# Optimization experiments

Measured on AMD Instinct MI355X. Metric: run time of the kernel, lower is better.

Reference implementation:

```python
import jax, jax.numpy as jnp
import numpy as np

B, N = 8, 2048
HYPER, IN_F, OUT_F = 128, 64, 64
ALPHA = 0.2  # LeakyReLU negative slope
NEG_INF = -9e15


def setup_inputs() -> dict:
    key = jax.random.key(0)
    k1, k2, k3, k4, k5, k6 = jax.random.split(key, 6)
    state = jax.random.normal(k1, (B, HYPER), dtype=jnp.float32)
    h = jax.random.normal(k2, (B, N, IN_F), dtype=jnp.float32)
    adj = jax.random.randint(k3, (B, N, N), 0, 2, dtype=jnp.int32)
    # hypernetwork linear: weight [in*out, hyper] (torch layout), bias [in*out]
    lim = 1.0 / np.sqrt(HYPER)
    Wp_w = jax.random.uniform(k4, (IN_F * OUT_F, HYPER), minval=-lim, maxval=lim, dtype=jnp.float32)
    Wp_b = jax.random.uniform(k5, (IN_F * OUT_F,), minval=-lim, maxval=lim, dtype=jnp.float32)
    # attention vector a [2*out, 1], xavier_uniform gain=1.414
    ga = 1.414 * np.sqrt(6.0 / (2 * OUT_F + 1))
    a = jax.random.uniform(k6, (2 * OUT_F, 1), minval=-ga, maxval=ga, dtype=jnp.float32)
    return {"state": state, "h": h, "adj": adj, "Wp_w": Wp_w, "Wp_b": Wp_b, "a": a}


def reference(state, h, adj, Wp_w, Wp_b, a):
    # hypernetwork-generated weight: abs(Linear(state)) -> [B, in, out]
    W = jnp.abs(state @ Wp_w.T + Wp_b).reshape(-1, IN_F, OUT_F)
    Wh = jnp.einsum('bni,bio->bno', h, W)          # [B, N, out]
    Wh1 = Wh @ a[:OUT_F, :]                        # [B, N, 1]
    Wh2 = Wh @ a[OUT_F:, :]                        # [B, N, 1]
    e = jax.nn.leaky_relu(Wh1 + jnp.transpose(Wh2, (0, 2, 1)), negative_slope=ALPHA)  # [B, N, N]
    scores = jnp.where(adj > 0, e, NEG_INF)
    attention = jax.nn.softmax(scores, axis=1)     # softmax over dim=1 as in original
    h_prime = jnp.einsum('bmn,bmo->bno', jnp.transpose(attention, (0, 2, 1)), Wh) if False else attention @ Wh
    return jax.nn.elu(h_prime)                     # concat=True
```

## Files before the change

### kernel.cpp

```cpp
#include <hip/hip_runtime.h>
#include <hip/hip_bf16.h>
#include <hip/hip_fp16.h>

#define B_ 8
#define N_ 2048
#define ALPHA_ 0.2f
#define LOG2E_ 1.44269504088896f

#define OFF_WB    0u
#define OFF_WA1   65536u
#define OFF_WA2   67584u
#define OFF_WH1   69632u
#define OFF_WH2   135168u
#define OFF_DEN   200704u
#define OFF_WHBT  266240u
#define OFF_MASK  2363392u

typedef _Float16 half8_t __attribute__((ext_vector_type(8)));
typedef float f32x4_t __attribute__((ext_vector_type(4)));
union UH { unsigned u[4]; half8_t s; };

__device__ __forceinline__ unsigned pkh(float a, float b) {
  __half2 h = __floats2half2_rn(a, b);
  return *(unsigned*)&h;
}
__device__ __forceinline__ unsigned pk2(float lo, float hi) {
  return ((__float_as_uint(hi) + 0x8000u) & 0xFFFF0000u) |
         ((__float_as_uint(lo) + 0x8000u) >> 16);
}

__global__ __launch_bounds__(256) void k1_hyperw(
    const float* __restrict__ state, const float* __restrict__ Wpw,
    const float* __restrict__ Wpb, const float* __restrict__ av,
    unsigned short* __restrict__ Wb, float* __restrict__ Wa1,
    float* __restrict__ Wa2) {
  int b = blockIdx.y;
  int r = blockIdx.x * 256 + threadIdx.x;
  int lane = threadIdx.x & 63;
  int i = r >> 6, o = r & 63;
  __shared__ float st[128];
  if (threadIdx.x < 128) st[threadIdx.x] = state[b * 128 + threadIdx.x];
  __syncthreads();
  float acc = Wpb[r];
  const float4* wp = (const float4*)(Wpw + (size_t)r * 128);
  #pragma unroll 8
  for (int hh = 0; hh < 32; ++hh) {
    float4 v = wp[hh];
    acc += st[hh*4]*v.x + st[hh*4+1]*v.y + st[hh*4+2]*v.z + st[hh*4+3]*v.w;
  }
  float wv = fabsf(acc);
  __half hw = __float2half(wv);
  Wb[b * 4096 + o * 64 + i] = *(unsigned short*)&hw;
  float p1 = wv * av[lane];
  float p2 = wv * av[64 + lane];
  #pragma unroll
  for (int off = 32; off > 0; off >>= 1) {
    p1 += __shfl_xor(p1, off);
    p2 += __shfl_xor(p2, off);
  }
  if (lane == 0) { Wa1[b * 64 + i] = p1; Wa2[b * 64 + i] = p2; }
}

__global__ __launch_bounds__(256) void k2_wh(
    const float* __restrict__ h, const unsigned short* __restrict__ Wb,
    const float* __restrict__ Wa1, const float* __restrict__ Wa2,
    float* __restrict__ Wh1, float* __restrict__ Wh2,
    unsigned short* __restrict__ WhbT) {
  int b = blockIdx.y;
  int tid = threadIdx.x, lane = tid & 63;
  int w = tid >> 6;
  int n0 = blockIdx.x * 64 + w * 16;
  int l15 = lane & 15, kg = lane >> 4;
  int row = n0 + l15;
  const float* hrow = h + (((size_t)b * N_ + row) << 6);
  float4 ha0 = *(const float4*)(hrow + kg * 8);
  float4 ha1 = *(const float4*)(hrow + kg * 8 + 4);
  float4 hb0 = *(const float4*)(hrow + 32 + kg * 8);
  float4 hb1 = *(const float4*)(hrow + 32 + kg * 8 + 4);
  const float* wa1 = Wa1 + b * 64;
  const float* wa2 = Wa2 + b * 64;
  float4 A0 = *(const float4*)(wa1 + kg * 8),      A1 = *(const float4*)(wa1 + kg * 8 + 4);
  float4 A2 = *(const float4*)(wa1 + 32 + kg * 8), A3 = *(const float4*)(wa1 + 32 + kg * 8 + 4);
  float4 C0 = *(const float4*)(wa2 + kg * 8),      C1 = *(const float4*)(wa2 + kg * 8 + 4);
  float4 C2 = *(const float4*)(wa2 + 32 + kg * 8), C3 = *(const float4*)(wa2 + 32 + kg * 8 + 4);
  float v1 = ha0.x*A0.x + ha0.y*A0.y + ha0.z*A0.z + ha0.w*A0.w
           + ha1.x*A1.x + ha1.y*A1.y + ha1.z*A1.z + ha1.w*A1.w
           + hb0.x*A2.x + hb0.y*A2.y + hb0.z*A2.z + hb0.w*A2.w
           + hb1.x*A3.x + hb1.y*A3.y + hb1.z*A3.z + hb1.w*A3.w;
  float v2 = ha0.x*C0.x + ha0.y*C0.y + ha0.z*C0.z + ha0.w*C0.w
           + ha1.x*C1.x + ha1.y*C1.y + ha1.z*C1.z + ha1.w*C1.w
           + hb0.x*C2.x + hb0.y*C2.y + hb0.z*C2.z + hb0.w*C2.w
           + hb1.x*C3.x + hb1.y*C3.y + hb1.z*C3.z + hb1.w*C3.w;
  v1 += __shfl_xor(v1, 16); v1 += __shfl_xor(v1, 32);
  v2 += __shfl_xor(v2, 16); v2 += __shfl_xor(v2, 32);
  if (lane < 16) {
    Wh1[b * N_ + row] = v1 * LOG2E_;
    Wh2[b * N_ + row] = v2 * LOG2E_;
  }
  UH ua, ub;
  ua.u[0] = pkh(ha0.x, ha0.y); ua.u[1] = pkh(ha0.z, ha0.w);
  ua.u[2] = pkh(ha1.x, ha1.y); ua.u[3] = pkh(ha1.z, ha1.w);
  ub.u[0] = pkh(hb0.x, hb0.y); ub.u[1] = pkh(hb0.z, hb0.w);
  ub.u[2] = pkh(hb1.x, hb1.y); ub.u[3] = pkh(hb1.z, hb1.w);
  const unsigned short* wbb = Wb + b * 4096;
  f32x4_t acc[4];
  #pragma unroll
  for (int of = 0; of < 4; ++of) acc[of] = {0.f, 0.f, 0.f, 0.f};
  #pragma unroll
  for (int of = 0; of < 4; ++of) {
    int o = of * 16 + l15;
    half8_t b0 = *(const half8_t*)(wbb + o * 64 + kg * 8);
    half8_t b1 = *(const half8_t*)(wbb + o * 64 + 32 + kg * 8);
    acc[of] = __builtin_amdgcn_mfma_f32_16x16x32_f16(ua.s, b0, acc[of], 0, 0, 0);
    acc[of] = __builtin_amdgcn_mfma_f32_16x16x32_f16(ub.s, b1, acc[of], 0, 0, 0);
  }
  int nb = n0 + (kg << 2);
  #pragma unroll
  for (int of = 0; of < 4; ++of) {
    int o = of * 16 + l15;
    uint2 pk;
    pk.x = pkh(acc[of][0], acc[of][1]);
    pk.y = pkh(acc[of][2], acc[of][3]);
    *(uint2*)(WhbT + ((size_t)(b * 64 + o)) * N_ + nb) = pk;
  }
}

#define K3_PROC(VV, UVV, II)                                                 \
  do {                                                                       \
    bool p0 = (VV).x > 0, p1 = (VV).y > 0, p2 = (VV).z > 0, p3 = (VV).w > 0; \
    unsigned long long b0 = __ballot(p0), b1 = __ballot(p1);                 \
    unsigned long long b2 = __ballot(p2), b3 = __ballot(p3);                 \
    unsigned long long bsel = qsel == 0 ? b0 : qsel == 1 ? b1                \
                            : qsel == 2 ? b2 : b3;                           \
    wreg = (rsel == (II)) ? bsel : wreg;                                     \
    den0 += p0 ? fmaxf((UVV).x, (UVV).y * b2c0) : 0.f;                       \
    den1 += p1 ? fmaxf((UVV).x, (UVV).y * b2c1) : 0.f;                       \
    den2 += p2 ? fmaxf((UVV).x, (UVV).y * b2c2) : 0.f;                       \
    den3 += p3 ? fmaxf((UVV).x, (UVV).y * b2c3) : 0.f;                       \
  } while (0)

__global__ __launch_bounds__(256) void k3_mask(
    const int* __restrict__ adj, const float* __restrict__ Wh1,
    const float* __restrict__ Wh2, float* __restrict__ den,
    unsigned long long* __restrict__ maskQ) {
  int jg = blockIdx.x, ic = blockIdx.y, b = blockIdx.z;
  int tid = threadIdx.x, lane = tid & 63, w = tid >> 6;
  int i0 = ic * 64 + w * 16;
  __shared__ float2 uvs[64];
  __shared__ float red[4][256];
  if (tid < 64) {
    float w1v = Wh1[b * N_ + ic * 64 + tid];
    uvs[tid] = make_float2(exp2f(w1v), exp2f(0.2f * w1v));
  }
  __syncthreads();
  float2 uv0 = uvs[(w<<4)+0],  uv1 = uvs[(w<<4)+1],  uv2 = uvs[(w<<4)+2],  uv3 = uvs[(w<<4)+3];
  float2 uv4 = uvs[(w<<4)+4],  uv5 = uvs[(w<<4)+5],  uv6 = uvs[(w<<4)+6],  uv7 = uvs[(w<<4)+7];
  float2 uv8 = uvs[(w<<4)+8],  uv9 = uvs[(w<<4)+9],  uvA = uvs[(w<<4)+10], uvB = uvs[(w<<4)+11];
  float2 uvC = uvs[(w<<4)+12], uvD = uvs[(w<<4)+13], uvE = uvs[(w<<4)+14], uvF = uvs[(w<<4)+15];
  int j0 = jg * 256 + 4 * lane;
  float4 wh2v = *(const float4*)(Wh2 + b * N_ + j0);
  float b2c0 = exp2f(-0.8f * wh2v.x), b2c1 = exp2f(-0.8f * wh2v.y);
  float b2c2 = exp2f(-0.8f * wh2v.z), b2c3 = exp2f(-0.8f * wh2v.w);
  const int4* ap = (const int4*)(adj + ((size_t)(b * N_ + i0)) * N_ + jg * 256);
  const size_t rs = N_ / 4;
  int qsel = lane & 3, rsel = lane >> 2;
  unsigned long long wreg = 0;
  float den0 = 0.f, den1 = 0.f, den2 = 0.f, den3 = 0.f;
  int4 r0 = ap[0 * rs + lane], r1 = ap[1 * rs + lane];
  int4 r2 = ap[2 * rs + lane], r3 = ap[3 * rs + lane];
  int4 r4 = ap[4 * rs + lane], r5 = ap[5 * rs + lane];
  int4 r6 = ap[6 * rs + lane], r7 = ap[7 * rs + lane];
  K3_PROC(r0, uv0, 0);  r0 = ap[8 * rs + lane];
  K3_PROC(r1, uv1, 1);  r1 = ap[9 * rs + lane];
  K3_PROC(r2, uv2, 2);  r2 = ap[10 * rs + lane];
  K3_PROC(r3, uv3, 3);  r3 = ap[11 * rs + lane];
  K3_PROC(r4, uv4, 4);  r4 = ap[12 * rs + lane];
  K3_PROC(r5, uv5, 5);  r5 = ap[13 * rs + lane];
  K3_PROC(r6, uv6, 6);  r6 = ap[14 * rs + lane];
  K3_PROC(r7, uv7, 7);  r7 = ap[15 * rs + lane];
  K3_PROC(r0, uv8, 8);  K3_PROC(r1, uv9, 9);  K3_PROC(r2, uvA, 10); K3_PROC(r3, uvB, 11);
  K3_PROC(r4, uvC, 12); K3_PROC(r5, uvD, 13); K3_PROC(r6, uvE, 14); K3_PROC(r7, uvF, 15);
  maskQ[((((size_t)b * 8 + jg) * 2048 + i0 + rsel) << 2) + qsel] = wreg;
  red[w][(lane << 2) + 0] = den0;
  red[w][(lane << 2) + 1] = den1;
  red[w][(lane << 2) + 2] = den2;
  red[w][(lane << 2) + 3] = den3;
  __syncthreads();
  float dsum = red[0][tid] + red[1][tid] + red[2][tid] + red[3][tid];
  atomicAdd(den + b * N_ + jg * 256 + tid, dsum);
}

__global__ __launch_bounds__(512) void k4_mfma(
    const unsigned long long* __restrict__ maskQ, const float* __restrict__ Wh1,
    const float* __restrict__ Wh2, const float* __restrict__ den,
    const unsigned short* __restrict__ WhbT, float* __restrict__ out) {
  int ib = blockIdx.x, b = blockIdx.y;
  int tid = threadIdx.x, lane = tid & 63;
  int w = __builtin_amdgcn_readfirstlane(tid >> 6);
  int iw = w & 3, kh = w >> 2;
  extern __shared__ __align__(16) unsigned char smem[];
  unsigned* abL = (unsigned*)(smem + 32768);
  const unsigned short* wsrc = WhbT + (size_t)b * 64 * N_;
  int sl1 = 512 + tid, sl2 = 1024 + tid, sl3 = 1536 + tid;
  int h0 = 0, h1 = 0, h2 = 1, h3 = 1;
  int o0 = tid >> 4, o1 = (sl1 & 1023) >> 4, o2 = (sl2 & 1023) >> 4, o3 = (sl3 & 1023) >> 4;
  int s0 = tid & 15, s1 = sl1 & 15, s2 = sl2 & 15, s3 = sl3 & 15;
  uint4 sv0, sv1, sv2, sv3;
#define SLOAD(RR)                                                               \
  { sv0 = *(const uint4*)(wsrc + (size_t)o0 * N_ + h0 * 1024 + (RR) * 128 + s0 * 8); \
    sv1 = *(const uint4*)(wsrc + (size_t)o1 * N_ + h1 * 1024 + (RR) * 128 + s1 * 8); \
    sv2 = *(const uint4*)(wsrc + (size_t)o2 * N_ + h2 * 1024 + (RR) * 128 + s2 * 8); \
    sv3 = *(const uint4*)(wsrc + (size_t)o3 * N_ + h3 * 1024 + (RR) * 128 + s3 * 8); }
#define SWRITE()                                                                \
  { *(uint4*)(smem + h0 * 16384 + o0 * 256 + ((s0 * 16) ^ ((o0 & 7) << 4))) = sv0; \
    *(uint4*)(smem + h1 * 16384 + o1 * 256 + ((s1 * 16) ^ ((o1 & 7) << 4))) = sv1; \
    *(uint4*)(smem + h2 * 16384 + o2 * 256 + ((s2 * 16) ^ ((o2 & 7) << 4))) = sv2; \
    *(uint4*)(smem + h3 * 16384 + o3 * 256 + ((s3 * 16) ^ ((o3 & 7) << 4))) = sv3; }
  SLOAD(0)
  #pragma unroll
  for (int q = 0; q < 4; ++q) {
    int j = (q << 9) + tid;
    float dv = den[b * N_ + j];
    float inv = 1.0f / fmaxf(dv, 1e-37f);
    float B4 = exp2f(-0.8f * Wh2[b * N_ + j]) * inv;
    abL[j] = pk2(B4, inv);
  }
  SWRITE()
  int l15 = lane & 15, lg = lane >> 4;
  int i0 = (ib << 6) + (iw << 4);
  int i = i0 + l15;
  float w1 = Wh1[b * N_ + i];
  float u = exp2f(w1), v = exp2f(0.2f * w1);
  f32x4_t acc[4];
  #pragma unroll
  for (int of = 0; of < 4; ++of) acc[of] = {0.f, 0.f, 0.f, 0.f};
  unsigned char* mybt = smem + kh * 16384;
  const unsigned long long* mbase = maskQ + (size_t)b * 8 * 2048 * 4;
  for (int rr = 0; rr < 8; ++rr) {
    __syncthreads();
    if (rr < 7) SLOAD(rr + 1)
    int tg = kh * 8 + rr;
    int jg = tg >> 1, r2 = tg & 1;
    const uint4* qp = (const uint4*)(mbase + (((size_t)jg * 2048 + i) << 2));
    uint4 q0 = qp[0], q1 = qp[1];
    unsigned long long Wq[4];
    Wq[0] = ((unsigned long long)q0.y << 32) | q0.x;
    Wq[1] = ((unsigned long long)q0.w << 32) | q0.z;
    Wq[2] = ((unsigned long long)q1.y << 32) | q1.x;
    Wq[3] = ((unsigned long long)q1.w << 32) | q1.z;
    #pragma unroll
    for (int jt2 = 0; jt2 < 2; ++jt2) {
      #pragma unroll
      for (int s = 0; s < 2; ++s) {
        int jfull = kh * 1024 + rr * 128 + jt2 * 64 + s * 32 + lg * 8;
        int tbase = r2 * 32 + jt2 * 16 + s * 8 + lg * 2;
        unsigned m[4];
        #pragma unroll
        for (int k2 = 0; k2 < 4; ++k2)
          m[k2] = (unsigned)(Wq[k2] >> tbase) & 3u;
        const uint4* abp = (const uint4*)&abL[jfull];
        uint4 a0 = abp[0], a1 = abp[1];
        unsigned aw[8] = {a0.x, a0.y, a0.z, a0.w, a1.x, a1.y, a1.z, a1.w};
        UH A;
        #pragma unroll
        for (int p2 = 0; p2 < 4; ++p2) {
          int e0 = 2 * p2, e1 = 2 * p2 + 1;
          float A40 = __uint_as_float(aw[e0] & 0xFFFF0000u);
          float B40 = __uint_as_float(aw[e0] << 16);
          float A41 = __uint_as_float(aw[e1] & 0xFFFF0000u);
          float B41 = __uint_as_float(aw[e1] << 16);
          float plo = fmaxf(u * A40, v * B40);
          float phi = fmaxf(u * A41, v * B41);
          plo = (m[e0 & 3] & (1u << (e0 >> 2))) ? plo : 0.f;
          phi = (m[e1 & 3] & (1u << (e1 >> 2))) ? phi : 0.f;
          A.u[p2] = pkh(plo, phi);
        }
        int boff = jt2 * 128 + s * 64 + lg * 16;
        #pragma unroll
        for (int of = 0; of < 4; ++of) {
          int o = (of << 4) + l15;
          half8_t bv = *(const half8_t*)(mybt + o * 256 + (boff ^ ((o & 7) << 4)));
          acc[of] = __builtin_amdgcn_mfma_f32_16x16x32_f16(A.s, bv, acc[of], 0, 0, 0);
        }
      }
    }
    __syncthreads();
    if (rr < 7) SWRITE()
  }
  __syncthreads();
  float* fred = (float*)smem;
  if (kh == 1) {
    #pragma unroll
    for (int of = 0; of < 4; ++of)
      *(f32x4_t*)(fred + (((iw << 6) + lane) << 4) + (of << 2)) = acc[of];
  }
  __syncthreads();
  if (kh == 0) {
    #pragma unroll
    for (int of = 0; of < 4; ++of) {
      f32x4_t oth = *(const f32x4_t*)(fred + (((iw << 6) + lane) << 4) + (of << 2));
      #pragma unroll
      for (int q = 0; q < 4; ++q) {
        float xv = acc[of][q] + oth[q];
        xv = xv > 0.f ? xv : (__expf(xv) - 1.f);
        out[((size_t)(b * N_ + i0 + (lg << 2) + q)) * 64 + (of << 4) + l15] = xv;
      }
    }
  }
}

extern "C" void kernel_launch(void* const* d_in, const int* in_sizes, int n_in,
                              void* d_out, int out_size, void* d_ws, size_t ws_size,
                              hipStream_t stream) {
  const float* state = (const float*)d_in[0];
  const float* h     = (const float*)d_in[1];
  const int*   adj   = (const int*)d_in[2];
  const float* Wpw   = (const float*)d_in[3];
  const float* Wpb   = (const float*)d_in[4];
  const float* av    = (const float*)d_in[5];
  float* out = (float*)d_out;
  char* ws = (char*)d_ws;
  unsigned short* Wb = (unsigned short*)(ws + OFF_WB);
  float* Wa1  = (float*)(ws + OFF_WA1);
  float* Wa2  = (float*)(ws + OFF_WA2);
  float* Wh1  = (float*)(ws + OFF_WH1);
  float* Wh2  = (float*)(ws + OFF_WH2);
  float* den  = (float*)(ws + OFF_DEN);
  unsigned short* WhbT = (unsigned short*)(ws + OFF_WHBT);
  unsigned long long* maskQ = (unsigned long long*)(ws + OFF_MASK);

  hipMemsetAsync(den, 0, B_ * N_ * sizeof(float), stream);
  hipLaunchKernelGGL(k1_hyperw, dim3(16, 8), dim3(256), 0, stream,
                     state, Wpw, Wpb, av, Wb, Wa1, Wa2);
  hipLaunchKernelGGL(k2_wh, dim3(32, 8), dim3(256), 0, stream,
                     h, Wb, Wa1, Wa2, Wh1, Wh2, WhbT);
  hipLaunchKernelGGL(k3_mask, dim3(8, 32, 8), dim3(256), 0, stream,
                     adj, Wh1, Wh2, den, maskQ);
  hipLaunchKernelGGL(k4_mfma, dim3(32, 8), dim3(512), 40960, stream,
                     maskQ, Wh1, Wh2, den, WhbT, out);
}
```

Measured before the change: 62.62 us.

## Retile k4 warps to 32x32 output tiles and fold den zeroing into k1

Each warp in the attention-aggregation kernel now computes a 32-row by 32-column output block instead of 16 rows by 64 columns. This lets each generated A fragment feed two MFMAs and halves the LDS B-fragment loads per MFMA, at the cost of computing attention weights for two row sets and loading two mask rows. Separately, the hipMemsetAsync of the denominator buffer is removed and the zeroing is done by the b==0 blocks of the first kernel. This saves one stream operation of launch overhead.

```diff
diff --git a/kernel.cpp b/kernel.cpp
--- a/kernel.cpp
+++ b/kernel.cpp
@@ -33,8 +33,13 @@
     const float* __restrict__ state, const float* __restrict__ Wpw,
     const float* __restrict__ Wpb, const float* __restrict__ av,
     unsigned short* __restrict__ Wb, float* __restrict__ Wa1,
-    float* __restrict__ Wa2) {
+    float* __restrict__ Wa2, float* __restrict__ den) {
   int b = blockIdx.y;
+  if (b == 0) {
+    int gid = blockIdx.x * 256 + threadIdx.x;
+    float4 z; z.x = 0.f; z.y = 0.f; z.z = 0.f; z.w = 0.f;
+    ((float4*)den)[gid] = z;
+  }
   int r = blockIdx.x * 256 + threadIdx.x;
   int lane = threadIdx.x & 63;
   int i = r >> 6, o = r & 63;
@@ -197,7 +202,7 @@
   int ib = blockIdx.x, b = blockIdx.y;
   int tid = threadIdx.x, lane = tid & 63;
   int w = __builtin_amdgcn_readfirstlane(tid >> 6);
-  int iw = w & 3, kh = w >> 2;
+  int os = w & 1, ip = (w >> 1) & 1, kh = w >> 2;
   extern __shared__ __align__(16) unsigned char smem[];
   unsigned* abL = (unsigned*)(smem + 32768);
   const unsigned short* wsrc = WhbT + (size_t)b * 64 * N_;
@@ -227,13 +232,14 @@
   }
   SWRITE()
   int l15 = lane & 15, lg = lane >> 4;
-  int i0 = (ib << 6) + (iw << 4);
-  int i = i0 + l15;
-  float w1 = Wh1[b * N_ + i];
-  float u = exp2f(w1), v = exp2f(0.2f * w1);
-  f32x4_t acc[4];
-  #pragma unroll
-  for (int of = 0; of < 4; ++of) acc[of] = {0.f, 0.f, 0.f, 0.f};
+  int i_a = (ib << 6) + (ip << 5) + l15;
+  int i_b = i_a + 16;
+  float w1a = Wh1[b * N_ + i_a], w1b = Wh1[b * N_ + i_b];
+  float u_a = exp2f(w1a), v_a = exp2f(0.2f * w1a);
+  float u_b = exp2f(w1b), v_b = exp2f(0.2f * w1b);
+  f32x4_t acc[2][2];
+  acc[0][0] = {0.f,0.f,0.f,0.f}; acc[0][1] = {0.f,0.f,0.f,0.f};
+  acc[1][0] = {0.f,0.f,0.f,0.f}; acc[1][1] = {0.f,0.f,0.f,0.f};
   unsigned char* mybt = smem + kh * 16384;
   const unsigned long long* mbase = maskQ + (size_t)b * 8 * 2048 * 4;
   for (int rr = 0; rr < 8; ++rr) {
@@ -241,27 +247,34 @@
     if (rr < 7) SLOAD(rr + 1)
     int tg = kh * 8 + rr;
     int jg = tg >> 1, r2 = tg & 1;
-    const uint4* qp = (const uint4*)(mbase + (((size_t)jg * 2048 + i) << 2));
-    uint4 q0 = qp[0], q1 = qp[1];
-    unsigned long long Wq[4];
-    Wq[0] = ((unsigned long long)q0.y << 32) | q0.x;
-    Wq[1] = ((unsigned long long)q0.w << 32) | q0.z;
-    Wq[2] = ((unsigned long long)q1.y << 32) | q1.x;
-    Wq[3] = ((unsigned long long)q1.w << 32) | q1.z;
+    const uint4* qpA = (const uint4*)(mbase + (((size_t)jg * 2048 + i_a) << 2));
+    const uint4* qpB = (const uint4*)(mbase + (((size_t)jg * 2048 + i_b) << 2));
+    uint4 a0 = qpA[0], a1 = qpA[1], b0 = qpB[0], b1 = qpB[1];
+    unsigned long long WqA[4], WqB[4];
+    WqA[0] = ((unsigned long long)a0.y << 32) | a0.x;
+    WqA[1] = ((unsigned long long)a0.w << 32) | a0.z;
+    WqA[2] = ((unsigned long long)a1.y << 32) | a1.x;
+    WqA[3] = ((unsigned long long)a1.w << 32) | a1.z;
+    WqB[0] = ((unsigned long long)b0.y << 32) | b0.x;
+    WqB[1] = ((unsigned long long)b0.w << 32) | b0.z;
+    WqB[2] = ((unsigned long long)b1.y << 32) | b1.x;
+    WqB[3] = ((unsigned long long)b1.w << 32) | b1.z;
     #pragma unroll
     for (int jt2 = 0; jt2 < 2; ++jt2) {
       #pragma unroll
       for (int s = 0; s < 2; ++s) {
         int jfull = kh * 1024 + rr * 128 + jt2 * 64 + s * 32 + lg * 8;
         int tbase = r2 * 32 + jt2 * 16 + s * 8 + lg * 2;
-        unsigned m[4];
+        unsigned mA[4], mB[4];
         #pragma unroll
-        for (int k2 = 0; k2 < 4; ++k2)
-          m[k2] = (unsigned)(Wq[k2] >> tbase) & 3u;
+        for (int k2 = 0; k2 < 4; ++k2) {
+          mA[k2] = (unsigned)(WqA[k2] >> tbase) & 3u;
+          mB[k2] = (unsigned)(WqB[k2] >> tbase) & 3u;
+        }
         const uint4* abp = (const uint4*)&abL[jfull];
-        uint4 a0 = abp[0], a1 = abp[1];
-        unsigned aw[8] = {a0.x, a0.y, a0.z, a0.w, a1.x, a1.y, a1.z, a1.w};
-        UH A;
+        uint4 q0 = abp[0], q1 = abp[1];
+        unsigned aw[8] = {q0.x, q0.y, q0.z, q0.w, q1.x, q1.y, q1.z, q1.w};
+        UH Aa, Ab;
         #pragma unroll
         for (int p2 = 0; p2 < 4; ++p2) {
           int e0 = 2 * p2, e1 = 2 * p2 + 1;
@@ -269,19 +282,27 @@
           float B40 = __uint_as_float(aw[e0] << 16);
           float A41 = __uint_as_float(aw[e1] & 0xFFFF0000u);
           float B41 = __uint_as_float(aw[e1] << 16);
-          float plo = fmaxf(u * A40, v * B40);
-          float phi = fmaxf(u * A41, v * B41);
-          plo = (m[e0 & 3] & (1u << (e0 >> 2))) ? plo : 0.f;
-          phi = (m[e1 & 3] & (1u << (e1 >> 2))) ? phi : 0.f;
-          A.u[p2] = pkh(plo, phi);
+          unsigned bm0 = 1u << (e0 >> 2), bm1 = 1u << (e1 >> 2);
+          float pa0 = fmaxf(u_a * A40, v_a * B40);
+          float pa1 = fmaxf(u_a * A41, v_a * B41);
+          pa0 = (mA[e0 & 3] & bm0) ? pa0 : 0.f;
+          pa1 = (mA[e1 & 3] & bm1) ? pa1 : 0.f;
+          Aa.u[p2] = pkh(pa0, pa1);
+          float pb0 = fmaxf(u_b * A40, v_b * B40);
+          float pb1 = fmaxf(u_b * A41, v_b * B41);
+          pb0 = (mB[e0 & 3] & bm0) ? pb0 : 0.f;
+          pb1 = (mB[e1 & 3] & bm1) ? pb1 : 0.f;
+          Ab.u[p2] = pkh(pb0, pb1);
         }
         int boff = jt2 * 128 + s * 64 + lg * 16;
-        #pragma unroll
-        for (int of = 0; of < 4; ++of) {
-          int o = (of << 4) + l15;
-          half8_t bv = *(const half8_t*)(mybt + o * 256 + (boff ^ ((o & 7) << 4)));
-          acc[of] = __builtin_amdgcn_mfma_f32_16x16x32_f16(A.s, bv, acc[of], 0, 0, 0);
-        }
+        int oc0 = (os << 5) + l15;
+        int oc1 = oc0 + 16;
+        half8_t bv0 = *(const half8_t*)(mybt + oc0 * 256 + (boff ^ ((oc0 & 7) << 4)));
+        half8_t bv1 = *(const half8_t*)(mybt + oc1 * 256 + (boff ^ ((oc1 & 7) << 4)));
+        acc[0][0] = __builtin_amdgcn_mfma_f32_16x16x32_f16(Aa.s, bv0, acc[0][0], 0, 0, 0);
+        acc[0][1] = __builtin_amdgcn_mfma_f32_16x16x32_f16(Aa.s, bv1, acc[0][1], 0, 0, 0);
+        acc[1][0] = __builtin_amdgcn_mfma_f32_16x16x32_f16(Ab.s, bv0, acc[1][0], 0, 0, 0);
+        acc[1][1] = __builtin_amdgcn_mfma_f32_16x16x32_f16(Ab.s, bv1, acc[1][1], 0, 0, 0);
       }
     }
     __syncthreads();
@@ -289,21 +310,29 @@
   }
   __syncthreads();
   float* fred = (float*)smem;
+  int grp = (ip << 1) | os;
   if (kh == 1) {
     #pragma unroll
-    for (int of = 0; of < 4; ++of)
-      *(f32x4_t*)(fred + (((iw << 6) + lane) << 4) + (of << 2)) = acc[of];
+    for (int f2 = 0; f2 < 2; ++f2)
+      #pragma unroll
+      for (int of = 0; of < 2; ++of)
+        *(f32x4_t*)(fred + ((grp * 64 + lane) << 4) + ((f2 * 2 + of) << 2)) = acc[f2][of];
   }
   __syncthreads();
   if (kh == 0) {
     #pragma unroll
-    for (int of = 0; of < 4; ++of) {
-      f32x4_t oth = *(const f32x4_t*)(fred + (((iw << 6) + lane) << 4) + (of << 2));
+    for (int f2 = 0; f2 < 2; ++f2) {
       #pragma unroll
-      for (int q = 0; q < 4; ++q) {
-        float xv = acc[of][q] + oth[q];
-        xv = xv > 0.f ? xv : (__expf(xv) - 1.f);
-        out[((size_t)(b * N_ + i0 + (lg << 2) + q)) * 64 + (of << 4) + l15] = xv;
+      for (int of = 0; of < 2; ++of) {
+        f32x4_t oth = *(const f32x4_t*)(fred + ((grp * 64 + lane) << 4) + ((f2 * 2 + of) << 2));
+        #pragma unroll
+        for (int q = 0; q < 4; ++q) {
+          float xv = acc[f2][of][q] + oth[q];
+          xv = xv > 0.f ? xv : (__expf(xv) - 1.f);
+          int row = (ib << 6) + (ip << 5) + (f2 << 4) + (lg << 2) + q;
+          int col = (os << 5) + (of << 4) + l15;
+          out[(((size_t)(b * N_ + row)) << 6) + col] = xv;
+        }
       }
     }
   }
@@ -329,9 +358,8 @@
   unsigned short* WhbT = (unsigned short*)(ws + OFF_WHBT);
   unsigned long long* maskQ = (unsigned long long*)(ws + OFF_MASK);
 
-  hipMemsetAsync(den, 0, B_ * N_ * sizeof(float), stream);
   hipLaunchKernelGGL(k1_hyperw, dim3(16, 8), dim3(256), 0, stream,
-                     state, Wpw, Wpb, av, Wb, Wa1, Wa2);
+                     state, Wpw, Wpb, av, Wb, Wa1, Wa2, den);
   hipLaunchKernelGGL(k2_wh, dim3(32, 8), dim3(256), 0, stream,
                      h, Wb, Wa1, Wa2, Wh1, Wh2, WhbT);
   hipLaunchKernelGGL(k3_mask, dim3(8, 32, 8), dim3(256), 0, stream,
```

Result: slower. 65.20 us (+4.1%).
